# Kernel optimization log

Hardware: AMD Instinct MI355X
Metric: run time of the kernel (lower is better)

## Reference

```python
import jax, jax.numpy as jnp
import numpy as np

B, S, D, H, HD = 2, 2048, 1024, 16, 64
SCALE = HD ** (-0.5)

def setup_inputs() -> dict:
    key = jax.random.key(0)
    ks = jax.random.split(key, 11)
    f = jax.random.normal
    return {
        "K_in": f(ks[0], (B, S, D), jnp.float32),
        "V_in": f(ks[1], (B, S, D), jnp.float32),
        "Q_in": f(ks[2], (B, S, D), jnp.float32),
        "Wk": f(ks[3], (H, D, HD), jnp.float32) * 0.02,
        "bk": f(ks[4], (H, HD), jnp.float32) * 0.02,
        "Wq": f(ks[5], (H, D, HD), jnp.float32) * 0.02,
        "bq": f(ks[6], (H, HD), jnp.float32) * 0.02,
        "Wv": f(ks[7], (H, D, HD), jnp.float32) * 0.02,
        "bv": f(ks[8], (H, HD), jnp.float32) * 0.02,
        "Wp": f(ks[9], (D, D), jnp.float32) * 0.02,
        "bp": f(ks[10], (D,), jnp.float32) * 0.02,
    }

def reference(K_in, V_in, Q_in, Wk, bk, Wq, bq, Wv, bv, Wp, bp):
    # Per-head linear projections (batched over heads): [B,H,S,HD]
    K = jnp.einsum('bsd,hde->bhse', K_in, Wk) + bk[None, :, None, :]
    Q = jnp.einsum('bsd,hde->bhse', Q_in, Wq) + bq[None, :, None, :]
    V = jnp.einsum('bsd,hde->bhse', V_in, Wv) + bv[None, :, None, :]
    # Attention scores [B,H,S,S], softmax over keys
    W = jax.nn.softmax(jnp.einsum('bhqe,bhke->bhqk', Q, K) * SCALE, axis=-1)
    val = jnp.einsum('bhqk,bhke->bhqe', W, V)            # [B,H,S,HD]
    # Concatenate heads along feature dim -> [B,S,H*HD] = [B,S,D]
    concat = jnp.transpose(val, (0, 2, 1, 3)).reshape(K_in.shape[0], K_in.shape[1], -1)
    return concat @ Wp.T + bp
```

## Files before the change

kernel.cpp:

```cpp
#include <hip/hip_runtime.h>
#include <hip/hip_bf16.h>
#include <math.h>

typedef float f32x4 __attribute__((ext_vector_type(4)));
typedef short s16x8 __attribute__((ext_vector_type(8)));
typedef unsigned short us16x4 __attribute__((ext_vector_type(4)));
typedef unsigned short us16x8 __attribute__((ext_vector_type(8)));
typedef unsigned int u32x2 __attribute__((ext_vector_type(2)));

#define MFMA16(a, b, c) __builtin_amdgcn_mfma_f32_16x16x32_bf16(a, b, c, 0, 0, 0)

static constexpr int B_ = 2, S_ = 2048, D_ = 1024, H_ = 16, HD_ = 64;
static constexpr float QSCALE = 0.125f * 1.44269504088896340736f;

__device__ __forceinline__ unsigned short f2bf(float f) {
    unsigned int u = __builtin_bit_cast(unsigned int, f);
    u += 0x7fffu + ((u >> 16) & 1);
    return (unsigned short)(u >> 16);
}

#if defined(__has_builtin) && __has_builtin(__builtin_amdgcn_cvt_pk_bf16_f32)
typedef __bf16 bf16x2v __attribute__((ext_vector_type(2)));
__device__ __forceinline__ unsigned int pk_bf16(float a, float b) {
    return __builtin_bit_cast(unsigned int, __builtin_amdgcn_cvt_pk_bf16_f32(a, b));
}
#else
__device__ __forceinline__ unsigned int pk_bf16(float a, float b) {
    return ((unsigned int)f2bf(a)) | (((unsigned int)f2bf(b)) << 16);
}
#endif

__device__ __forceinline__ void glds16(const unsigned short* g, unsigned short* l) {
    __builtin_amdgcn_global_load_lds(
        (const __attribute__((address_space(1))) void*)g,
        (__attribute__((address_space(3))) void*)l, 16, 0, 0);
}

__global__ __launch_bounds__(256) void conv3(const float* __restrict__ s0,
                                             const float* __restrict__ s1,
                                             const float* __restrict__ s2,
                                             unsigned short* __restrict__ d0,
                                             unsigned short* __restrict__ d1,
                                             unsigned short* __restrict__ d2) {
    const int z = blockIdx.z;
    const float* src = (z == 0) ? s0 : (z == 1) ? s1 : s2;
    unsigned short* dst = (z == 0) ? d0 : (z == 1) ? d1 : d2;
    int i = (blockIdx.x * 256 + threadIdx.x) * 8;
    f32x4 a = *(const f32x4*)&src[i];
    f32x4 b = *(const f32x4*)&src[i + 4];
    s16x8 o;
#pragma unroll
    for (int j = 0; j < 4; j++) { o[j] = (short)f2bf(a[j]); o[4 + j] = (short)f2bf(b[j]); }
    *(s16x8*)&dst[i] = o;
}

__global__ __launch_bounds__(256) void conv_bf16(const float* __restrict__ src,
                                                 unsigned short* __restrict__ dst) {
    int i = (blockIdx.x * 256 + threadIdx.x) * 8;
    f32x4 a = *(const f32x4*)&src[i];
    f32x4 b = *(const f32x4*)&src[i + 4];
    s16x8 o;
#pragma unroll
    for (int j = 0; j < 4; j++) { o[j] = (short)f2bf(a[j]); o[4 + j] = (short)f2bf(b[j]); }
    *(s16x8*)&dst[i] = o;
}

__global__ __launch_bounds__(256) void transpose_w3(const float* __restrict__ W0,
                                                    const float* __restrict__ W1,
                                                    const float* __restrict__ W2,
                                                    unsigned short* __restrict__ Wt3) {
    const int z = blockIdx.z;
    const float* W = (z == 0) ? W0 : (z == 1) ? W1 : W2;
    unsigned short* dst = Wt3 + ((size_t)z << 20);
    const int h = blockIdx.x >> 2, dg = blockIdx.x & 3;
    const int lane = threadIdx.x & 63, w = threadIdx.x >> 6;
    const float* Wh = W + ((size_t)h << 16);
#pragma unroll
    for (int it = 0; it < 8; it++) {
        int d0 = dg * 256 + it * 32 + w * 8;
        us16x8 o;
#pragma unroll
        for (int j = 0; j < 8; j++) o[j] = f2bf(Wh[(d0 + j) * 64 + lane]);
        *(us16x8*)&dst[(size_t)(h * 64 + lane) * 1024 + d0] = o;
    }
}

__device__ __forceinline__ void gemm_core128(const unsigned short* __restrict__ A,
                                             const unsigned short* __restrict__ Bt,
                                             unsigned short* As, unsigned short* Bs,
                                             int m0, int n0, f32x4 acc[4][4]) {
    const int tid = threadIdx.x;
    const int lane = tid & 63;
    const int w = tid >> 6, wm = w & 1, wn = w >> 1;
    const int l16 = lane & 15, quad = lane >> 4;
    const int srow = tid >> 3;
    const int sg = (tid & 7) ^ (srow & 7);
    const unsigned short* Ag = A + (size_t)(m0 + srow) * 1024 + sg * 8;
    const unsigned short* Bg = Bt + (size_t)(n0 + srow) * 1024 + sg * 8;
    unsigned short* Al = As + tid * 8;
    unsigned short* Bl = Bs + tid * 8;
    const int xo = (l16 & 7);

    for (int k0 = 0; k0 < 1024; k0 += 64) {
        __syncthreads();
#pragma unroll
        for (int c = 0; c < 4; c++) {
            glds16(Ag + (size_t)c * 32 * 1024 + k0, Al + c * 2048);
            glds16(Bg + (size_t)c * 32 * 1024 + k0, Bl + c * 2048);
        }
        __syncthreads();
#pragma unroll
        for (int kc = 0; kc < 2; kc++) {
            s16x8 bf[4];
#pragma unroll
            for (int nt = 0; nt < 4; nt++)
                bf[nt] = *(const s16x8*)&Bs[(wn * 64 + nt * 16 + l16) * 64 +
                                            (((kc * 4 + quad) ^ xo) * 8)];
#pragma unroll
            for (int mt = 0; mt < 4; mt++) {
                s16x8 af = *(const s16x8*)&As[(wm * 64 + mt * 16 + l16) * 64 +
                                              (((kc * 4 + quad) ^ xo) * 8)];
#pragma unroll
                for (int nt = 0; nt < 4; nt++)
                    acc[mt][nt] = MFMA16(af, bf[nt], acc[mt][nt]);
            }
        }
    }
}

__global__ __launch_bounds__(256) void gemm_qkv(const unsigned short* __restrict__ Qc,
                                                const unsigned short* __restrict__ Kc,
                                                const unsigned short* __restrict__ Vc,
                                                const unsigned short* __restrict__ Wt3,
                                                const float* __restrict__ bq,
                                                const float* __restrict__ bk,
                                                const float* __restrict__ bv,
                                                unsigned short* __restrict__ Qr,
                                                unsigned short* __restrict__ Kr,
                                                unsigned short* __restrict__ Vt) {
    __shared__ unsigned short As[128 * 64];
    __shared__ unsigned short Bs[128 * 64];
    const int z = blockIdx.z;
    const unsigned short* A = (z == 0) ? Qc : (z == 1) ? Kc : Vc;
    const unsigned short* Bt = Wt3 + ((size_t)z << 20);
    const float* bias = (z == 0) ? bq : (z == 1) ? bk : bv;
    const int m0 = blockIdx.y * 128, n0 = blockIdx.x * 128;

    f32x4 acc[4][4] = {};
    gemm_core128(A, Bt, As, Bs, m0, n0, acc);

    const int tid = threadIdx.x;
    const int lane = tid & 63, w = tid >> 6;
    const int wm = w & 1, wn = w >> 1;
    const int l16 = lane & 15, quad = lane >> 4;
    const float scl = (z == 0) ? QSCALE : 1.0f;

    __syncthreads();
    unsigned short* T = ((w < 2) ? As : Bs) + (w & 1) * 4096;
#pragma unroll
    for (int mt = 0; mt < 4; mt++)
#pragma unroll
        for (int nt = 0; nt < 4; nt++) {
            int nl = nt * 16 + l16;
            float bsv = bias[n0 + wn * 64 + nl];
#pragma unroll
            for (int r = 0; r < 4; r++) {
                int ml = mt * 16 + quad * 4 + r;
                unsigned short val = f2bf((acc[mt][nt][r] + bsv) * scl);
                int row = (z == 2) ? nl : ml;
                int col = (z == 2) ? ml : nl;
                T[row * 64 + (((col >> 3) ^ (row & 7)) * 8) + (col & 7)] = val;
            }
        }
#pragma unroll
    for (int it = 0; it < 8; it++) {
        int rr = it * 8 + (lane >> 3);
        int g = lane & 7;
        us16x8 vv = *(const us16x8*)&T[rr * 64 + ((g ^ (rr & 7)) * 8)];
        if (z == 2) {
            int n = n0 + wn * 64 + rr;
            int mb = m0 + wm * 64 + g * 8;
            int b = mb >> 11, s = mb & 2047;
            *(us16x8*)&Vt[(((size_t)(b * H_ + (n >> 6))) * HD_ + (n & 63)) * S_ + s] = vv;
        } else {
            unsigned short* dst = z ? Kr : Qr;
            *(us16x8*)&dst[(size_t)(m0 + wm * 64 + rr) * 1024 + n0 + wn * 64 + g * 8] = vv;
        }
    }
}

__global__ __launch_bounds__(256) void gemm_out(const unsigned short* __restrict__ A,
                                                const unsigned short* __restrict__ Bt,
                                                const float* __restrict__ bias,
                                                float* __restrict__ C) {
    __shared__ unsigned short As[128 * 64];
    __shared__ unsigned short Bs[64 * 64];
    const int tid = threadIdx.x;
    const int lane = tid & 63;
    const int w = tid >> 6, wm = w & 1, wn = w >> 1;
    const int l16 = lane & 15, quad = lane >> 4;
    const int m0 = blockIdx.y * 128, n0 = blockIdx.x * 64;
    const int srow = tid >> 3;
    const int sg = (tid & 7) ^ (srow & 7);
    const unsigned short* Ag = A + (size_t)(m0 + srow) * 1024 + sg * 8;
    const unsigned short* Bg = Bt + (size_t)(n0 + srow) * 1024 + sg * 8;
    unsigned short* Al = As + tid * 8;
    unsigned short* Bl = Bs + tid * 8;
    const int xo = l16 & 7;

    f32x4 acc[4][2] = {};
    for (int k0 = 0; k0 < 1024; k0 += 64) {
        __syncthreads();
#pragma unroll
        for (int c = 0; c < 4; c++)
            glds16(Ag + (size_t)c * 32 * 1024 + k0, Al + c * 2048);
#pragma unroll
        for (int c = 0; c < 2; c++)
            glds16(Bg + (size_t)c * 32 * 1024 + k0, Bl + c * 2048);
        __syncthreads();
#pragma unroll
        for (int kc = 0; kc < 2; kc++) {
            s16x8 bf[2];
#pragma unroll
            for (int nt = 0; nt < 2; nt++)
                bf[nt] = *(const s16x8*)&Bs[(wn * 32 + nt * 16 + l16) * 64 +
                                            (((kc * 4 + quad) ^ xo) * 8)];
#pragma unroll
            for (int mt = 0; mt < 4; mt++) {
                s16x8 af = *(const s16x8*)&As[(wm * 64 + mt * 16 + l16) * 64 +
                                              (((kc * 4 + quad) ^ xo) * 8)];
#pragma unroll
                for (int nt = 0; nt < 2; nt++)
                    acc[mt][nt] = MFMA16(af, bf[nt], acc[mt][nt]);
            }
        }
    }
    const int lq = quad;
#pragma unroll
    for (int mt = 0; mt < 4; mt++)
#pragma unroll
        for (int nt = 0; nt < 2; nt++)
#pragma unroll
            for (int r = 0; r < 4; r++) {
                int mg = m0 + wm * 64 + mt * 16 + lq * 4 + r;
                int ng = n0 + wn * 32 + nt * 16 + l16;
                C[(size_t)mg * 1024 + ng] = acc[mt][nt][r] + bias[ng];
            }
}

__global__ __launch_bounds__(256) void flash_attn(const unsigned short* __restrict__ Qr,
                                                  const unsigned short* __restrict__ Kr,
                                                  const unsigned short* __restrict__ Vt,
                                                  unsigned short* __restrict__ Cc) {
    __shared__ unsigned short Ks[2][64 * 64];
    __shared__ unsigned short Vs[64 * 64];
    constexpr int LDT = 72;
    __shared__ unsigned short P4[4][16 * LDT];

    const int tid = threadIdx.x;
    const int lane = tid & 63, w = tid >> 6;
    const int l16 = lane & 15, quad = lane >> 4;
    const int bh = blockIdx.x, q0 = blockIdx.y * 64;
    const int b = bh >> 4, h = bh & 15;
    const int s_q = q0 + w * 16 + l16;

    const unsigned short* Qp = Qr + ((size_t)(b * S_ + s_q)) * D_ + h * HD_;

    const int srow = tid >> 3;
    const int sg = (tid & 7) ^ (srow & 7);
    const unsigned short* kg = Kr + ((size_t)(b * S_ + srow)) * D_ + h * HD_ + sg * 8;
    const unsigned short* vg = Vt + (((size_t)(b * H_ + h)) * HD_ + srow) * S_ + sg * 8;
    unsigned short* Vl = Vs + tid * 8;
    unsigned short* Pw = P4[w];
    const int pbase = l16 * LDT + quad * 4;
    const int xo = l16 & 7;

    glds16(kg, &Ks[0][tid * 8]);
    glds16(kg + (size_t)32 * D_, &Ks[0][tid * 8 + 2048]);
    kg += (size_t)64 * D_;

    s16x8 aq0 = *(const s16x8*)&Qp[quad * 8];
    s16x8 aq1 = *(const s16x8*)&Qp[32 + quad * 8];

    float l_part = 0.f;
    f32x4 o[4] = {};
    const f32x4 z4 = {0.f, 0.f, 0.f, 0.f};

    asm volatile("s_waitcnt vmcnt(0) lgkmcnt(0)\n\ts_barrier" ::: "memory");

    int cur = 0;
    for (int t = 0; t < 32; ++t) {
        const int last = (t == 31);
        glds16(vg, Vl);
        glds16(vg + (size_t)32 * S_, Vl + 2048);
        vg += 64;
        if (!last) {
            unsigned short* Kn = &Ks[cur ^ 1][tid * 8];
            glds16(kg, Kn);
            glds16(kg + (size_t)32 * D_, Kn + 2048);
            kg += (size_t)64 * D_;
        }

        const unsigned short* Kc_ = &Ks[cur][0];
        __builtin_amdgcn_s_setprio(1);
#pragma unroll
        for (int g = 0; g < 4; g++) {
            int row = g * 16 + l16;
            s16x8 kb0 = *(const s16x8*)&Kc_[row * 64 + ((quad ^ xo) * 8)];
            s16x8 kb1 = *(const s16x8*)&Kc_[row * 64 + (((4 + quad) ^ xo) * 8)];
            f32x4 sc = MFMA16(kb0, aq0, z4);
            sc = MFMA16(kb1, aq1, sc);
            float e0 = exp2f(sc[0]), e1 = exp2f(sc[1]);
            float e2 = exp2f(sc[2]), e3 = exp2f(sc[3]);
            l_part += (e0 + e1) + (e2 + e3);
            u32x2 pv;
            pv[0] = pk_bf16(e0, e1);
            pv[1] = pk_bf16(e2, e3);
            *(u32x2*)&Pw[pbase + g * 16] = pv;
        }
        __builtin_amdgcn_s_setprio(0);
        s16x8 pB0 = *(const s16x8*)&Pw[l16 * LDT + quad * 8];
        s16x8 pB1 = *(const s16x8*)&Pw[l16 * LDT + 32 + quad * 8];

        if (!last)
            asm volatile("s_waitcnt vmcnt(2)\n\ts_barrier" ::: "memory");
        else
            asm volatile("s_waitcnt vmcnt(0)\n\ts_barrier" ::: "memory");

        __builtin_amdgcn_s_setprio(1);
#pragma unroll
        for (int tt = 0; tt < 4; tt++) {
            int row = tt * 16 + l16;
            s16x8 v0 = *(const s16x8*)&Vs[row * 64 + ((quad ^ xo) * 8)];
            s16x8 v1 = *(const s16x8*)&Vs[row * 64 + (((4 + quad) ^ xo) * 8)];
            o[tt] = MFMA16(v0, pB0, o[tt]);
            o[tt] = MFMA16(v1, pB1, o[tt]);
        }
        __builtin_amdgcn_s_setprio(0);
        asm volatile("s_waitcnt vmcnt(0) lgkmcnt(0)\n\ts_barrier" ::: "memory");
        cur ^= 1;
    }

    float l = l_part;
    l += __shfl_xor(l, 16);
    l += __shfl_xor(l, 32);
    float rinv = 1.0f / l;
    unsigned short* Cp = Cc + ((size_t)(b * S_ + s_q)) * D_ + h * HD_;
#pragma unroll
    for (int t = 0; t < 4; t++) {
        u32x2 ov;
        ov[0] = pk_bf16(o[t][0] * rinv, o[t][1] * rinv);
        ov[1] = pk_bf16(o[t][2] * rinv, o[t][3] * rinv);
        *(u32x2*)&Cp[t * 16 + quad * 4] = ov;
    }
}

extern "C" void kernel_launch(void* const* d_in, const int* in_sizes, int n_in,
                              void* d_out, int out_size, void* d_ws, size_t ws_size,
                              hipStream_t stream) {
    const float* K_in = (const float*)d_in[0];
    const float* V_in = (const float*)d_in[1];
    const float* Q_in = (const float*)d_in[2];
    const float* Wk   = (const float*)d_in[3];
    const float* bk   = (const float*)d_in[4];
    const float* Wq   = (const float*)d_in[5];
    const float* bq   = (const float*)d_in[6];
    const float* Wv   = (const float*)d_in[7];
    const float* bv   = (const float*)d_in[8];
    const float* Wp   = (const float*)d_in[9];
    const float* bp   = (const float*)d_in[10];

    unsigned short* ws16 = (unsigned short*)d_ws;
    const size_t MC = 1u << 20;
    unsigned short* Qc  = ws16;
    unsigned short* Kc  = Qc + 4 * MC;
    unsigned short* Vc  = Kc + 4 * MC;
    unsigned short* Wt3 = Vc + 4 * MC;
    unsigned short* Qr  = Wt3 + 3 * MC;
    unsigned short* Kr  = Qr + 4 * MC;
    unsigned short* Vt  = Kr + 4 * MC;
    unsigned short* Cc  = Qc;
    unsigned short* Wpb = Wt3;

    conv3<<<dim3(2048, 1, 3), 256, 0, stream>>>(Q_in, K_in, V_in, Qc, Kc, Vc);
    transpose_w3<<<dim3(64, 1, 3), 256, 0, stream>>>(Wq, Wk, Wv, Wt3);

    gemm_qkv<<<dim3(8, 32, 3), 256, 0, stream>>>(Qc, Kc, Vc, Wt3, bq, bk, bv, Qr, Kr, Vt);

    conv_bf16<<<512, 256, 0, stream>>>(Wp, Wpb);

    flash_attn<<<dim3(32, 32), 256, 0, stream>>>(Qr, Kr, Vt, Cc);

    gemm_out<<<dim3(16, 32), 256, 0, stream>>>(Cc, Wpb, bp, (float*)d_out);
}
```

Before: 260.0 us.

## Split attention warps into 2x2 query/key grid with cross-warp output reduction

Each warp now covers 32 queries against half of each 64-key tile instead of 16 queries against the full tile. This lets each loaded K and V fragment feed two MFMAs, reducing LDS reads per MFMA. The two key-halves' partial outputs and row sums are combined at the end through shared memory, reusing the K and V buffers. The cost is more accumulator registers and an extra reduction phase with two block barriers.

```diff
diff --git a/kernel.cpp b/kernel.cpp
--- a/kernel.cpp
+++ b/kernel.cpp
@@ -254,17 +254,22 @@
                                                   unsigned short* __restrict__ Cc) {
     __shared__ unsigned short Ks[2][64 * 64];
     __shared__ unsigned short Vs[64 * 64];
-    constexpr int LDT = 72;
-    __shared__ unsigned short P4[4][16 * LDT];
+    constexpr int LDT = 36;
+    __shared__ unsigned short P4[4][32 * LDT];
 
     const int tid = threadIdx.x;
     const int lane = tid & 63, w = tid >> 6;
     const int l16 = lane & 15, quad = lane >> 4;
+    const int qh = w & 1, kh = w >> 1;
     const int bh = blockIdx.x, q0 = blockIdx.y * 64;
     const int b = bh >> 4, h = bh & 15;
-    const int s_q = q0 + w * 16 + l16;
-
-    const unsigned short* Qp = Qr + ((size_t)(b * S_ + s_q)) * D_ + h * HD_;
+
+    const unsigned short* Qp0 = Qr + ((size_t)(b * S_ + q0 + qh * 32 + l16)) * D_ + h * HD_;
+    s16x8 aq[2][2];
+    aq[0][0] = *(const s16x8*)&Qp0[quad * 8];
+    aq[0][1] = *(const s16x8*)&Qp0[32 + quad * 8];
+    aq[1][0] = *(const s16x8*)&Qp0[(size_t)16 * D_ + quad * 8];
+    aq[1][1] = *(const s16x8*)&Qp0[(size_t)16 * D_ + 32 + quad * 8];
 
     const int srow = tid >> 3;
     const int sg = (tid & 7) ^ (srow & 7);
@@ -272,18 +277,14 @@
     const unsigned short* vg = Vt + (((size_t)(b * H_ + h)) * HD_ + srow) * S_ + sg * 8;
     unsigned short* Vl = Vs + tid * 8;
     unsigned short* Pw = P4[w];
-    const int pbase = l16 * LDT + quad * 4;
     const int xo = l16 & 7;
 
     glds16(kg, &Ks[0][tid * 8]);
     glds16(kg + (size_t)32 * D_, &Ks[0][tid * 8 + 2048]);
     kg += (size_t)64 * D_;
 
-    s16x8 aq0 = *(const s16x8*)&Qp[quad * 8];
-    s16x8 aq1 = *(const s16x8*)&Qp[32 + quad * 8];
-
-    float l_part = 0.f;
-    f32x4 o[4] = {};
+    float l_part[2] = {0.f, 0.f};
+    f32x4 o[2][4] = {};
     const f32x4 z4 = {0.f, 0.f, 0.f, 0.f};
 
     asm volatile("s_waitcnt vmcnt(0) lgkmcnt(0)\n\ts_barrier" ::: "memory");
@@ -304,23 +305,26 @@
         const unsigned short* Kc_ = &Ks[cur][0];
         __builtin_amdgcn_s_setprio(1);
 #pragma unroll
-        for (int g = 0; g < 4; g++) {
-            int row = g * 16 + l16;
+        for (int kg16 = 0; kg16 < 2; kg16++) {
+            int row = kh * 32 + kg16 * 16 + l16;
             s16x8 kb0 = *(const s16x8*)&Kc_[row * 64 + ((quad ^ xo) * 8)];
             s16x8 kb1 = *(const s16x8*)&Kc_[row * 64 + (((4 + quad) ^ xo) * 8)];
-            f32x4 sc = MFMA16(kb0, aq0, z4);
-            sc = MFMA16(kb1, aq1, sc);
-            float e0 = exp2f(sc[0]), e1 = exp2f(sc[1]);
-            float e2 = exp2f(sc[2]), e3 = exp2f(sc[3]);
-            l_part += (e0 + e1) + (e2 + e3);
-            u32x2 pv;
-            pv[0] = pk_bf16(e0, e1);
-            pv[1] = pk_bf16(e2, e3);
-            *(u32x2*)&Pw[pbase + g * 16] = pv;
+#pragma unroll
+            for (int qf = 0; qf < 2; qf++) {
+                f32x4 sc = MFMA16(kb0, aq[qf][0], z4);
+                sc = MFMA16(kb1, aq[qf][1], sc);
+                float e0 = exp2f(sc[0]), e1 = exp2f(sc[1]);
+                float e2 = exp2f(sc[2]), e3 = exp2f(sc[3]);
+                l_part[qf] += (e0 + e1) + (e2 + e3);
+                u32x2 pv;
+                pv[0] = pk_bf16(e0, e1);
+                pv[1] = pk_bf16(e2, e3);
+                *(u32x2*)&Pw[(qf * 16 + l16) * LDT + kg16 * 16 + quad * 4] = pv;
+            }
         }
         __builtin_amdgcn_s_setprio(0);
         s16x8 pB0 = *(const s16x8*)&Pw[l16 * LDT + quad * 8];
-        s16x8 pB1 = *(const s16x8*)&Pw[l16 * LDT + 32 + quad * 8];
+        s16x8 pB1 = *(const s16x8*)&Pw[(16 + l16) * LDT + quad * 8];
 
         if (!last)
             asm volatile("s_waitcnt vmcnt(2)\n\ts_barrier" ::: "memory");
@@ -331,27 +335,57 @@
 #pragma unroll
         for (int tt = 0; tt < 4; tt++) {
             int row = tt * 16 + l16;
-            s16x8 v0 = *(const s16x8*)&Vs[row * 64 + ((quad ^ xo) * 8)];
-            s16x8 v1 = *(const s16x8*)&Vs[row * 64 + (((4 + quad) ^ xo) * 8)];
-            o[tt] = MFMA16(v0, pB0, o[tt]);
-            o[tt] = MFMA16(v1, pB1, o[tt]);
+            s16x8 v = *(const s16x8*)&Vs[row * 64 + (((kh * 4 + quad) ^ xo) * 8)];
+            o[0][tt] = MFMA16(v, pB0, o[0][tt]);
+            o[1][tt] = MFMA16(v, pB1, o[1][tt]);
         }
         __builtin_amdgcn_s_setprio(0);
         asm volatile("s_waitcnt vmcnt(0) lgkmcnt(0)\n\ts_barrier" ::: "memory");
         cur ^= 1;
     }
 
-    float l = l_part;
-    l += __shfl_xor(l, 16);
-    l += __shfl_xor(l, 32);
-    float rinv = 1.0f / l;
-    unsigned short* Cp = Cc + ((size_t)(b * S_ + s_q)) * D_ + h * HD_;
-#pragma unroll
-    for (int t = 0; t < 4; t++) {
-        u32x2 ov;
-        ov[0] = pk_bf16(o[t][0] * rinv, o[t][1] * rinv);
-        ov[1] = pk_bf16(o[t][2] * rinv, o[t][3] * rinv);
-        *(u32x2*)&Cp[t * 16 + quad * 4] = ov;
+    __syncthreads();
+    float* Ored = (float*)Ks;
+    float* Lred = (float*)Vs;
+    float lw[2];
+#pragma unroll
+    for (int qf = 0; qf < 2; qf++) {
+        float l = l_part[qf];
+        l += __shfl_xor(l, 16);
+        l += __shfl_xor(l, 32);
+        lw[qf] = l;
+    }
+    if (kh == 1) {
+#pragma unroll
+        for (int qf = 0; qf < 2; qf++) {
+#pragma unroll
+            for (int tt = 0; tt < 4; tt++)
+#pragma unroll
+                for (int r = 0; r < 4; r++)
+                    Ored[qh * 2048 + (tt * 16 + quad * 4 + r) * 32 + qf * 16 + l16] =
+                        o[qf][tt][r];
+            if (quad == 0) Lred[qh * 32 + qf * 16 + l16] = lw[qf];
+        }
+    }
+    __syncthreads();
+    if (kh == 0) {
+#pragma unroll
+        for (int qf = 0; qf < 2; qf++) {
+            float rinv = 1.0f / (lw[qf] + Lred[qh * 32 + qf * 16 + l16]);
+            const int s_q = q0 + qh * 32 + qf * 16 + l16;
+            unsigned short* Cp = Cc + ((size_t)(b * S_ + s_q)) * D_ + h * HD_;
+#pragma unroll
+            for (int tt = 0; tt < 4; tt++) {
+                float s0 = o[qf][tt][0] + Ored[qh * 2048 + (tt * 16 + quad * 4 + 0) * 32 + qf * 16 + l16];
+                float s1 = o[qf][tt][1] + Ored[qh * 2048 + (tt * 16 + quad * 4 + 1) * 32 + qf * 16 + l16];
+                float s2 = o[qf][tt][2] + Ored[qh * 2048 + (tt * 16 + quad * 4 + 2) * 32 + qf * 16 + l16];
+                float s3 = o[qf][tt][3] + Ored[qh * 2048 + (tt * 16 + quad * 4 + 3) * 32 + qf * 16 + l16];
+                u32x2 ov;
+                ov[0] = pk_bf16(s0 * rinv, s1 * rinv);
+                ov[1] = pk_bf16(s2 * rinv, s3 * rinv);
+                *(u32x2*)&Cp[tt * 16 + quad * 4] = ov;
+            }
+        }
     }
 }
 
```

Measured after the change: 259.9 us. Within noise of the previous version (-0.0%).
